# Kernel tuning notes

Hardware: AMD Instinct MI355X
Metric: run time of the kernel (lower is better)

Reference implementation:

```python
import jax, jax.numpy as jnp
import numpy as np

LN_EPS = 1e-5   # torch LayerNorm default
EPS = 1e-8      # slot-attention renorm eps
ITERS = 3


def _ln(x, g, b):
    m = jnp.mean(x, axis=-1, keepdims=True)
    v = jnp.mean(jnp.square(x - m), axis=-1, keepdims=True)
    return (x - m) * jax.lax.rsqrt(v + LN_EPS) * g + b


def _gru(x, h, W_ih, W_hh, b_ih, b_hh):
    # torch GRUCell: gates ordered r, z, n; weight_* has shape [3h, in]
    gi = x @ W_ih.T + b_ih
    gh = h @ W_hh.T + b_hh
    ir, iz, inn = jnp.split(gi, 3, axis=-1)
    hr, hz, hn = jnp.split(gh, 3, axis=-1)
    r = jax.nn.sigmoid(ir + hr)
    z = jax.nn.sigmoid(iz + hz)
    n = jnp.tanh(inn + r * hn)
    return (1.0 - z) * n + z * h


def setup_inputs() -> dict:
    key = jax.random.key(0)
    ks = jax.random.split(key, 16)
    b, n, d, n_s = 32, 4096, 256, 8
    h = max(d, 128)  # hidden_dim = max(dim, hidden_dim)
    s = 1.0 / np.sqrt(d)
    inp = {
        "inputs": jax.random.normal(ks[0], (b, n, d), jnp.float32),
        "noise": jax.random.normal(ks[1], (b, n_s, d), jnp.float32),
        "slots_mu": jax.random.normal(ks[2], (1, 1, d), jnp.float32),
        "slots_logsigma": jax.random.normal(ks[3], (1, 1, d), jnp.float32) * 0.1,
        "Wq": jax.random.uniform(ks[4], (d, d), jnp.float32, -s, s),
        "bq": jnp.zeros((d,), jnp.float32),
        "Wk": jax.random.uniform(ks[5], (d, d), jnp.float32, -s, s),
        "bk": jnp.zeros((d,), jnp.float32),
        "Wv": jax.random.uniform(ks[6], (d, d), jnp.float32, -s, s),
        "bv": jnp.zeros((d,), jnp.float32),
        "W_ih": jax.random.uniform(ks[7], (3 * d, d), jnp.float32, -s, s),
        "W_hh": jax.random.uniform(ks[8], (3 * d, d), jnp.float32, -s, s),
        "b_ih": jnp.zeros((3 * d,), jnp.float32),
        "b_hh": jnp.zeros((3 * d,), jnp.float32),
        "W1": jax.random.uniform(ks[9], (h, d), jnp.float32, -s, s),
        "b1": jnp.zeros((h,), jnp.float32),
        "W2": jax.random.uniform(ks[10], (d, h), jnp.float32, -s, s),
        "b2": jnp.zeros((d,), jnp.float32),
        "g_in": jnp.ones((d,), jnp.float32), "be_in": jnp.zeros((d,), jnp.float32),
        "g_sl": jnp.ones((d,), jnp.float32), "be_sl": jnp.zeros((d,), jnp.float32),
        "g_ff": jnp.ones((d,), jnp.float32), "be_ff": jnp.zeros((d,), jnp.float32),
    }
    return inp


def reference(inputs, noise, slots_mu, slots_logsigma, Wq, bq, Wk, bk, Wv, bv,
              W_ih, W_hh, b_ih, b_hh, W1, b1, W2, b2,
              g_in, be_in, g_sl, be_sl, g_ff, be_ff):
    b, n, d = inputs.shape
    scale = d ** (-0.5)
    # reparameterized slot init
    slots = slots_mu + jnp.exp(slots_logsigma) * noise          # [b, n_s, d]
    x = _ln(inputs, g_in, be_in)
    k = x @ Wk.T + bk                                           # [b, n, d]
    v = x @ Wv.T + bv
    attn = None
    for _ in range(ITERS):
        slots_prev = slots
        q = _ln(slots, g_sl, be_sl) @ Wq.T + bq                 # [b, n_s, d]
        dots = jnp.einsum('bid,bjd->bij', q, k) * scale         # [b, n_s, n]
        attn = jax.nn.softmax(dots, axis=1)                     # softmax over SLOTS
        attn_ = attn + EPS
        attn_ = attn_ / jnp.sum(attn_, axis=-1, keepdims=True)  # renorm over inputs
        updates = jnp.einsum('bjd,bij->bid', v, attn_)          # [b, n_s, d]
        slots = _gru(updates.reshape(-1, d), slots_prev.reshape(-1, d),
                     W_ih, W_hh, b_ih, b_hh).reshape(b, -1, d)
        pre = _ln(slots, g_ff, be_ff)
        slots = slots + (jax.nn.relu(pre @ W1.T + b1) @ W2.T + b2)
    return (slots, attn)
```

## Files before the change

kernel.cpp:

```cpp
#include <hip/hip_runtime.h>
#include <hip/hip_fp16.h>
#include <cstdint>
#include <cstddef>


#define NTOK 4096
#define DDIM 256
#define NSLOT 8
#define NBATCH 32
#define CH 32
#define NCHK 128
#define SROWS (NBATCH * NSLOT)
#define NROWS (NBATCH * NTOK)
#define SCALE 0.0625f
#define LN_EPS_C 1e-5f
#define ATTN_EPS_C 1e-8f

__device__ __forceinline__ void wave_reduce2(float& s, float& ss) {
#pragma unroll
  for (int off = 32; off > 0; off >>= 1) {
    s  += __shfl_down(s, off, 64);
    ss += __shfl_down(ss, off, 64);
  }
}
__device__ __forceinline__ void wave_reduce2_xor(float& s, float& ss) {
#pragma unroll
  for (int off = 32; off > 0; off >>= 1) {
    s  += __shfl_xor(s, off, 64);
    ss += __shfl_xor(ss, off, 64);
  }
}

__global__ __launch_bounds__(256) void convert_weights_k(
    const float* __restrict__ Wq, const float* __restrict__ Wv,
    const float* __restrict__ Wih, const float* __restrict__ Whh,
    const float* __restrict__ W1, const float* __restrict__ W2,
    const float* __restrict__ Wk, __half* __restrict__ WqT,
    __half* __restrict__ WvT, __half* __restrict__ WihT,
    __half* __restrict__ WhhT, __half* __restrict__ W1T,
    __half* __restrict__ W2T, __half* __restrict__ Wk_h) {
  __shared__ float tile[32][33];
  int bz = blockIdx.x;
  int tx = threadIdx.x & 31, ty = threadIdx.x >> 5;
  if (bz >= 80) {
    int ro = (bz - 80) * 32, cd = blockIdx.y * 32;
#pragma unroll
    for (int p = 0; p < 32; p += 8)
      Wk_h[(size_t)(ro + ty + p) * DDIM + cd + tx] =
          __float2half(Wk[(size_t)(ro + ty + p) * DDIM + cd + tx]);
    return;
  }
  const float* in; __half* out; int O, bo;
  if (bz < 8)       { in = Wq;  out = WqT;  O = 256; bo = bz; }
  else if (bz < 16) { in = Wv;  out = WvT;  O = 256; bo = bz - 8; }
  else if (bz < 40) { in = Wih; out = WihT; O = 768; bo = bz - 16; }
  else if (bz < 64) { in = Whh; out = WhhT; O = 768; bo = bz - 40; }
  else if (bz < 72) { in = W1;  out = W1T;  O = 256; bo = bz - 64; }
  else              { in = W2;  out = W2T;  O = 256; bo = bz - 72; }
  int ro = bo * 32, cd = blockIdx.y * 32;
#pragma unroll
  for (int p = 0; p < 32; p += 8)
    tile[ty + p][tx] = in[(size_t)(ro + ty + p) * DDIM + cd + tx];
  __syncthreads();
#pragma unroll
  for (int p = 0; p < 32; p += 8)
    out[(size_t)(cd + ty + p) * O + ro + tx] = __float2half(tile[tx][ty + p]);
}

__global__ __launch_bounds__(256) void xh_prep_k(
    const float* __restrict__ X, const float* __restrict__ g,
    const float* __restrict__ be, __half* __restrict__ xh) {
  int row = blockIdx.x * 4 + (threadIdx.x >> 6);
  int lane = threadIdx.x & 63;
  float4 a = *(const float4*)(X + (size_t)row * DDIM + lane * 4);
  float s = a.x + a.y + a.z + a.w;
  float ss = a.x * a.x + a.y * a.y + a.z * a.z + a.w * a.w;
  wave_reduce2_xor(s, ss);
  float m = s * (1.f / DDIM);
  float rs = rsqrtf(ss * (1.f / DDIM) - m * m + LN_EPS_C);
  float4 gv = *(const float4*)(g + lane * 4);
  float4 bev = *(const float4*)(be + lane * 4);
  union { __half2 h[2]; uint2 u; } pk;
  pk.h[0] = __floats2half2_rn((a.x - m) * rs * gv.x + bev.x,
                              (a.y - m) * rs * gv.y + bev.y);
  pk.h[1] = __floats2half2_rn((a.z - m) * rs * gv.z + bev.z,
                              (a.w - m) * rs * gv.w + bev.w);
  *(uint2*)(xh + (size_t)row * DDIM + lane * 4) = pk.u;
}

__global__ __launch_bounds__(256) void fused_attn_f16_k(
    const __half* __restrict__ xh, const float* __restrict__ qk,
    const float* __restrict__ qkb, float* __restrict__ attn_out,
    float* __restrict__ S_part, __half* __restrict__ u_part, int write_attn) {
  __shared__ __half sx[CH][258];
  __shared__ float2 sqkf[NSLOT][128];
  __shared__ float part[4][NSLOT][CH];
  __shared__ float sa[NSLOT][CH];
  __shared__ float sC0[NSLOT], sS[NSLOT];
  int b = blockIdx.x, c = blockIdx.y, t = threadIdx.x;
  {
    int i = t >> 5, p2 = t & 31;
    const float* qr = qk + ((size_t)b * NSLOT + i) * DDIM;
#pragma unroll
    for (int kk = 0; kk < 4; ++kk) {
      int col = p2 * 4 + kk;
      sqkf[i][col] = make_float2(qr[col * 2], qr[col * 2 + 1]);
    }
  }
  if (t < NSLOT) sC0[t] = qkb[b * NSLOT + t];
  const size_t base = (size_t)b * NTOK + (size_t)c * CH;
#pragma unroll
  for (int it = 0; it < 4; ++it) {
    int e = it * 256 + t;
    int row = e >> 5, c16 = e & 31;
    uint4 v = *(const uint4*)(xh + (base + row) * DDIM + c16 * 8);
    __half2* dst = (__half2*)&sx[row][c16 * 8];
    dst[0] = ((const __half2*)&v)[0];
    dst[1] = ((const __half2*)&v)[1];
    dst[2] = ((const __half2*)&v)[2];
    dst[3] = ((const __half2*)&v)[3];
  }
  __syncthreads();
  int tj = t & 31, qd = t >> 5;
  float p[NSLOT] = {};
  const __half2* xrow = (const __half2*)&sx[tj][qd * 32];
#pragma unroll
  for (int dd2 = 0; dd2 < 16; ++dd2) {
    float2 xf = __half22float2(xrow[dd2]);
#pragma unroll
    for (int i = 0; i < NSLOT; ++i) {
      float2 qf = sqkf[i][qd * 16 + dd2];
      p[i] = fmaf(xf.x, qf.x, fmaf(xf.y, qf.y, p[i]));
    }
  }
#pragma unroll
  for (int i = 0; i < NSLOT; ++i) p[i] += __shfl_down(p[i], 32, 64);
  int w = t >> 6;
  if ((t & 63) < 32) {
#pragma unroll
    for (int i = 0; i < NSLOT; ++i) part[w][i][tj] = p[i];
  }
  __syncthreads();
  if (t < CH) {
    float dots[NSLOT], mx = -1e30f;
#pragma unroll
    for (int i = 0; i < NSLOT; ++i) {
      dots[i] = part[0][i][t] + part[1][i][t] + part[2][i][t] +
                part[3][i][t] + sC0[i];
      mx = fmaxf(mx, dots[i]);
    }
    float sum = 0.f;
#pragma unroll
    for (int i = 0; i < NSLOT; ++i) { dots[i] = expf(dots[i] - mx); sum += dots[i]; }
    float inv = 1.f / sum;
#pragma unroll
    for (int i = 0; i < NSLOT; ++i) {
      float a = dots[i] * inv;
      if (write_attn)
        attn_out[((size_t)b * NSLOT + i) * NTOK + c * CH + t] = a;
      float ae = a + ATTN_EPS_C;
      sa[i][t] = ae;
      float ps = ae;
#pragma unroll
      for (int off = 16; off > 0; off >>= 1) ps += __shfl_down(ps, off, 32);
      if (t == 0) sS[i] = ps;
    }
  }
  __syncthreads();
  float acc[NSLOT] = {};
#pragma unroll
  for (int jj = 0; jj < CH; ++jj) {
    float x = __half2float(sx[jj][t]);
#pragma unroll
    for (int i = 0; i < NSLOT; ++i) acc[i] = fmaf(x, sa[i][jj], acc[i]);
  }
  __half* upb = u_part + (((size_t)b * NCHK + c) * NSLOT) * DDIM + t;
#pragma unroll
  for (int i = 0; i < NSLOT; ++i) upb[(size_t)i * DDIM] = __float2half(acc[i]);
  if (t < NSLOT) S_part[((size_t)b * NCHK + c) * NSLOT + t] = sS[t];
}

__global__ __launch_bounds__(1024) void slot_update_k(
    const __half* __restrict__ u_part, const float* __restrict__ S_part,
    const float* __restrict__ slots_in, const __half* __restrict__ WvT,
    const float* __restrict__ bv, const __half* __restrict__ WihT,
    const __half* __restrict__ WhhT, const float* __restrict__ b_ih,
    const float* __restrict__ b_hh, const float* __restrict__ g_ff,
    const float* __restrict__ be_ff, const __half* __restrict__ W1T,
    const float* __restrict__ b1, const __half* __restrict__ W2T,
    const float* __restrict__ b2, const float* __restrict__ g_sl,
    const float* __restrict__ be_sl, const __half* __restrict__ WqT,
    const float* __restrict__ bq, const __half* __restrict__ Wk_h,
    const float* __restrict__ bk, const float* __restrict__ noise,
    const float* __restrict__ mu, const float* __restrict__ logsig,
    float* __restrict__ slots_out, float* __restrict__ qk,
    float* __restrict__ qkb_out, int init, int compute_qk) {
  __shared__ float red[4][6][DDIM];
  __shared__ float su[DDIM], sh[DDIM], supd[DDIM], v1[DDIM], v2[DDIM];
  __shared__ float scal[16];
  int r = blockIdx.x, t = threadIdx.x;
  int b = r >> 3, i = r & 7;
  int o = t & 255, ks = t >> 8;
  int lane = t & 63, wid = t >> 6;
  if (init) {
    if (ks == 0) {
      float ns = mu[o] + expf(logsig[o]) * noise[(size_t)r * DDIM + o];
      slots_out[(size_t)r * DDIM + o] = ns;
      v2[o] = ns;
    }
    __syncthreads();
  } else {
    {
      float up = 0.f;
      const __half* upp =
          u_part + (((size_t)b * NCHK + ks * 32) * NSLOT + i) * DDIM + o;
#pragma unroll
      for (int cc = 0; cc < 32; ++cc)
        up += __half2float(upp[(size_t)cc * (NSLOT * DDIM)]);
      red[ks][0][o] = up;
    }
    if (t < 128) {
      float sp = S_part[((size_t)b * NCHK + t) * NSLOT + i];
#pragma unroll
      for (int off = 32; off > 0; off >>= 1) sp += __shfl_down(sp, off, 64);
      if ((t & 63) == 0) scal[12 + (t >> 6)] = sp;
    }
    if (ks == 0) sh[o] = slots_in[(size_t)r * DDIM + o];
    __syncthreads();
    if (ks == 0) {
      float invS = 1.f / (scal[12] + scal[13]);
      su[o] = (red[0][0][o] + red[1][0][o] + red[2][0][o] + red[3][0][o]) * invS;
    }
    __syncthreads();
    {
      float p = 0.f;
      const __half* wp = WvT + (size_t)(ks * 64) * DDIM + o;
#pragma unroll 8
      for (int dd = 0; dd < 64; ++dd)
        p = fmaf(su[ks * 64 + dd], __half2float(wp[(size_t)dd * DDIM]), p);
      red[ks][0][o] = p;
    }
    __syncthreads();
    if (ks == 0)
      supd[o] = bv[o] + red[0][0][o] + red[1][0][o] + red[2][0][o] + red[3][0][o];
    __syncthreads();
    {
      float p0 = 0, p1 = 0, p2 = 0, p3 = 0, p4 = 0, p5 = 0;
      const __half* pi = WihT + (size_t)(ks * 64) * (3 * DDIM) + o;
      const __half* ph = WhhT + (size_t)(ks * 64) * (3 * DDIM) + o;
#pragma unroll 4
      for (int dd = 0; dd < 64; ++dd) {
        float ud = supd[ks * 64 + dd], hd = sh[ks * 64 + dd];
        size_t off = (size_t)dd * (3 * DDIM);
        p0 = fmaf(ud, __half2float(pi[off]), p0);
        p1 = fmaf(ud, __half2float(pi[off + DDIM]), p1);
        p2 = fmaf(ud, __half2float(pi[off + 2 * DDIM]), p2);
        p3 = fmaf(hd, __half2float(ph[off]), p3);
        p4 = fmaf(hd, __half2float(ph[off + DDIM]), p4);
        p5 = fmaf(hd, __half2float(ph[off + 2 * DDIM]), p5);
      }
      red[ks][0][o] = p0; red[ks][1][o] = p1; red[ks][2][o] = p2;
      red[ks][3][o] = p3; red[ks][4][o] = p4; red[ks][5][o] = p5;
    }
    __syncthreads();
    if (ks == 0) {
      float air = b_ih[o] + red[0][0][o] + red[1][0][o] + red[2][0][o] + red[3][0][o];
      float aiz = b_ih[DDIM + o] + red[0][1][o] + red[1][1][o] + red[2][1][o] + red[3][1][o];
      float ain = b_ih[2 * DDIM + o] + red[0][2][o] + red[1][2][o] + red[2][2][o] + red[3][2][o];
      float ahr = b_hh[o] + red[0][3][o] + red[1][3][o] + red[2][3][o] + red[3][3][o];
      float ahz = b_hh[DDIM + o] + red[0][4][o] + red[1][4][o] + red[2][4][o] + red[3][4][o];
      float ahn = b_hh[2 * DDIM + o] + red[0][5][o] + red[1][5][o] + red[2][5][o] + red[3][5][o];
      float rg = 1.f / (1.f + expf(-(air + ahr)));
      float zg = 1.f / (1.f + expf(-(aiz + ahz)));
      float ng = tanhf(ain + rg * ahn);
      float nh = (1.f - zg) * ng + zg * sh[o];
      v1[o] = nh;
      float s2 = nh, ss2 = nh * nh;
      wave_reduce2(s2, ss2);
      if (lane == 0) { scal[wid] = s2; scal[4 + wid] = ss2; }
    }
    __syncthreads();
    if (ks == 0) {
      float sS = scal[0] + scal[1] + scal[2] + scal[3];
      float sQ = scal[4] + scal[5] + scal[6] + scal[7];
      float m = sS * (1.f / DDIM);
      float rs = rsqrtf(sQ * (1.f / DDIM) - m * m + LN_EPS_C);
      v2[o] = (v1[o] - m) * rs * g_ff[o] + be_ff[o];
    }
    __syncthreads();
    {
      float p = 0.f;
      const __half* wp = W1T + (size_t)(ks * 64) * DDIM + o;
#pragma unroll 8
      for (int dd = 0; dd < 64; ++dd)
        p = fmaf(v2[ks * 64 + dd], __half2float(wp[(size_t)dd * DDIM]), p);
      red[ks][0][o] = p;
    }
    __syncthreads();
    if (ks == 0)
      su[o] = fmaxf(b1[o] + red[0][0][o] + red[1][0][o] + red[2][0][o] + red[3][0][o], 0.f);
    __syncthreads();
    {
      float p = 0.f;
      const __half* wp = W2T + (size_t)(ks * 64) * DDIM + o;
#pragma unroll 8
      for (int dd = 0; dd < 64; ++dd)
        p = fmaf(su[ks * 64 + dd], __half2float(wp[(size_t)dd * DDIM]), p);
      red[ks][0][o] = p;
    }
    __syncthreads();
    if (ks == 0) {
      float out = v1[o] + b2[o] + red[0][0][o] + red[1][0][o] + red[2][0][o] + red[3][0][o];
      slots_out[(size_t)r * DDIM + o] = out;
      v2[o] = out;
    }
    __syncthreads();
  }
  if (!compute_qk) return;
  if (ks == 0) {
    float x = v2[o];
    float s2 = x, ss2 = x * x;
    wave_reduce2(s2, ss2);
    if (lane == 0) { scal[wid] = s2; scal[4 + wid] = ss2; }
  }
  __syncthreads();
  if (ks == 0) {
    float sS = scal[0] + scal[1] + scal[2] + scal[3];
    float sQ = scal[4] + scal[5] + scal[6] + scal[7];
    float m = sS * (1.f / DDIM);
    float rs = rsqrtf(sQ * (1.f / DDIM) - m * m + LN_EPS_C);
    su[o] = (v2[o] - m) * rs * g_sl[o] + be_sl[o];
  }
  __syncthreads();
  {
    float p = 0.f;
    const __half* wp = WqT + (size_t)(ks * 64) * DDIM + o;
#pragma unroll 8
    for (int dd = 0; dd < 64; ++dd)
      p = fmaf(su[ks * 64 + dd], __half2float(wp[(size_t)dd * DDIM]), p);
    red[ks][0][o] = p;
  }
  __syncthreads();
  if (ks == 0)
    sh[o] = bq[o] + red[0][0][o] + red[1][0][o] + red[2][0][o] + red[3][0][o];
  __syncthreads();
  {
    float p = 0.f;
    const __half* wp = Wk_h + (size_t)(ks * 64) * DDIM + o;
#pragma unroll 8
    for (int dd = 0; dd < 64; ++dd)
      p = fmaf(sh[ks * 64 + dd], __half2float(wp[(size_t)dd * DDIM]), p);
    red[ks][0][o] = p;
  }
  __syncthreads();
  if (ks == 0) {
    float qkv = SCALE * (red[0][0][o] + red[1][0][o] + red[2][0][o] + red[3][0][o]);
    qk[(size_t)r * DDIM + o] = qkv;
    float v0 = sh[o] * bk[o], d1 = 0.f;
    wave_reduce2(v0, d1);
    if (lane == 0) scal[wid] = v0;
  }
  __syncthreads();
  if (t == 0)
    qkb_out[r] = SCALE * (scal[0] + scal[1] + scal[2] + scal[3]);
}

extern "C" void kernel_launch(void* const* d_in, const int* in_sizes, int n_in,
                              void* d_out, int out_size, void* d_ws,
                              size_t ws_size, hipStream_t stream) {
  const float* inputs   = (const float*)d_in[0];
  const float* noise    = (const float*)d_in[1];
  const float* slots_mu = (const float*)d_in[2];
  const float* slots_ls = (const float*)d_in[3];
  const float* Wq   = (const float*)d_in[4];
  const float* bq   = (const float*)d_in[5];
  const float* Wk   = (const float*)d_in[6];
  const float* bk   = (const float*)d_in[7];
  const float* Wv   = (const float*)d_in[8];
  const float* bv   = (const float*)d_in[9];
  const float* W_ih = (const float*)d_in[10];
  const float* W_hh = (const float*)d_in[11];
  const float* b_ih = (const float*)d_in[12];
  const float* b_hh = (const float*)d_in[13];
  const float* W1   = (const float*)d_in[14];
  const float* b1   = (const float*)d_in[15];
  const float* W2   = (const float*)d_in[16];
  const float* b2   = (const float*)d_in[17];
  const float* g_in = (const float*)d_in[18];
  const float* be_in= (const float*)d_in[19];
  const float* g_sl = (const float*)d_in[20];
  const float* be_sl= (const float*)d_in[21];
  const float* g_ff = (const float*)d_in[22];
  const float* be_ff= (const float*)d_in[23];

  float* out_slots = (float*)d_out;
  float* out_attn  = (float*)d_out + SROWS * DDIM;

  float* w = (float*)d_ws;
  float* slots = w;  w += SROWS * DDIM;
  float* qk = w;     w += SROWS * DDIM;
  float* qkb = w;    w += SROWS;
  float* S_part = w; w += NBATCH * NCHK * NSLOT;
  __half* h = (__half*)w;
  __half* xh = h;     h += (size_t)NROWS * DDIM;
  __half* u_part = h; h += (size_t)NBATCH * NCHK * NSLOT * DDIM;
  __half* WqT_h = h;  h += DDIM * DDIM;
  __half* WvT_h = h;  h += DDIM * DDIM;
  __half* WihT_h = h; h += DDIM * 3 * DDIM;
  __half* WhhT_h = h; h += DDIM * 3 * DDIM;
  __half* W1T_h = h;  h += DDIM * DDIM;
  __half* W2T_h = h;  h += DDIM * DDIM;
  __half* Wk_h = h;   h += DDIM * DDIM;

  convert_weights_k<<<dim3(88, 8), 256, 0, stream>>>(
      Wq, Wv, W_ih, W_hh, W1, W2, Wk, WqT_h, WvT_h, WihT_h, WhhT_h, W1T_h,
      W2T_h, Wk_h);
  slot_update_k<<<SROWS, 1024, 0, stream>>>(
      u_part, S_part, slots, WvT_h, bv, WihT_h, WhhT_h, b_ih, b_hh, g_ff,
      be_ff, W1T_h, b1, W2T_h, b2, g_sl, be_sl, WqT_h, bq, Wk_h, bk, noise,
      slots_mu, slots_ls, slots, qk, qkb, 1, 1);
  xh_prep_k<<<NROWS / 4, 256, 0, stream>>>(inputs, g_in, be_in, xh);
  for (int it = 0; it < 3; ++it) {
    fused_attn_f16_k<<<dim3(NBATCH, NCHK), 256, 0, stream>>>(
        xh, qk, qkb, out_attn, S_part, u_part, (it == 2) ? 1 : 0);
    float* sout = (it == 2) ? out_slots : slots;
    slot_update_k<<<SROWS, 1024, 0, stream>>>(
        u_part, S_part, slots, WvT_h, bv, WihT_h, WhhT_h, b_ih, b_hh, g_ff,
        be_ff, W1T_h, b1, W2T_h, b2, g_sl, be_sl, WqT_h, bq, Wk_h, bk, noise,
        slots_mu, slots_ls, sout, qk, qkb, 0, (it == 2) ? 0 : 1);
  }
}
```

Measured before the change: 247.2 us.

## Double attention chunk size and compute two token rows per thread

Raises the tokens per attention block from 32 to 64, halving the number of chunks and the per-chunk partial updates and normaliser sums written out. Each thread now holds two token rows in registers and reuses each float4 q vector loaded from shared memory for both dot products. The slot update kernel is adjusted to reduce over the smaller number of partials. The cost is more shared memory and registers per block, half as many blocks, and a reuse of scal[0] that could clash with other uses of that slot.

```diff
diff --git a/kernel.cpp b/kernel.cpp
--- a/kernel.cpp
+++ b/kernel.cpp
@@ -8,8 +8,8 @@
 #define DDIM 256
 #define NSLOT 8
 #define NBATCH 32
-#define CH 32
-#define NCHK 128
+#define CH 64
+#define NCHK 64
 #define SROWS (NBATCH * NSLOT)
 #define NROWS (NBATCH * NTOK)
 #define SCALE 0.0625f
@@ -93,24 +93,21 @@
     const float* __restrict__ qkb, float* __restrict__ attn_out,
     float* __restrict__ S_part, __half* __restrict__ u_part, int write_attn) {
   __shared__ __half sx[CH][258];
-  __shared__ float2 sqkf[NSLOT][128];
+  __shared__ float4 sq4[NSLOT][64];
   __shared__ float part[4][NSLOT][CH];
   __shared__ float sa[NSLOT][CH];
   __shared__ float sC0[NSLOT], sS[NSLOT];
   int b = blockIdx.x, c = blockIdx.y, t = threadIdx.x;
-  {
-    int i = t >> 5, p2 = t & 31;
-    const float* qr = qk + ((size_t)b * NSLOT + i) * DDIM;
-#pragma unroll
-    for (int kk = 0; kk < 4; ++kk) {
-      int col = p2 * 4 + kk;
-      sqkf[i][col] = make_float2(qr[col * 2], qr[col * 2 + 1]);
-    }
+#pragma unroll
+  for (int r2 = 0; r2 < 2; ++r2) {
+    int idx = r2 * 256 + t;
+    int i = idx >> 6, quad = idx & 63;
+    sq4[i][quad] = *(const float4*)(qk + ((size_t)b * NSLOT + i) * DDIM + quad * 4);
   }
   if (t < NSLOT) sC0[t] = qkb[b * NSLOT + t];
   const size_t base = (size_t)b * NTOK + (size_t)c * CH;
 #pragma unroll
-  for (int it = 0; it < 4; ++it) {
+  for (int it = 0; it < 8; ++it) {
     int e = it * 256 + t;
     int row = e >> 5, c16 = e & 31;
     uint4 v = *(const uint4*)(xh + (base + row) * DDIM + c16 * 8);
@@ -121,24 +118,33 @@
     dst[3] = ((const __half2*)&v)[3];
   }
   __syncthreads();
-  int tj = t & 31, qd = t >> 5;
-  float p[NSLOT] = {};
-  const __half2* xrow = (const __half2*)&sx[tj][qd * 32];
-#pragma unroll
-  for (int dd2 = 0; dd2 < 16; ++dd2) {
-    float2 xf = __half22float2(xrow[dd2]);
+  {
+    int tj = t & 31, qd = t >> 5;
+    float2 xa[16], xb[16];
+    const __half2* xra = (const __half2*)&sx[tj][qd * 32];
+    const __half2* xrb = (const __half2*)&sx[tj + 32][qd * 32];
+#pragma unroll
+    for (int d2 = 0; d2 < 16; ++d2) {
+      xa[d2] = __half22float2(xra[d2]);
+      xb[d2] = __half22float2(xrb[d2]);
+    }
+    int w = t >> 6;
+    bool lo = (t & 63) < 32;
 #pragma unroll
     for (int i = 0; i < NSLOT; ++i) {
-      float2 qf = sqkf[i][qd * 16 + dd2];
-      p[i] = fmaf(xf.x, qf.x, fmaf(xf.y, qf.y, p[i]));
-    }
-  }
-#pragma unroll
-  for (int i = 0; i < NSLOT; ++i) p[i] += __shfl_down(p[i], 32, 64);
-  int w = t >> 6;
-  if ((t & 63) < 32) {
-#pragma unroll
-    for (int i = 0; i < NSLOT; ++i) part[w][i][tj] = p[i];
+      float pa = 0.f, pb = 0.f;
+#pragma unroll
+      for (int d4 = 0; d4 < 8; ++d4) {
+        float4 q = sq4[i][qd * 8 + d4];
+        pa = fmaf(xa[2 * d4].x, q.x, fmaf(xa[2 * d4].y, q.y,
+             fmaf(xa[2 * d4 + 1].x, q.z, fmaf(xa[2 * d4 + 1].y, q.w, pa))));
+        pb = fmaf(xb[2 * d4].x, q.x, fmaf(xb[2 * d4].y, q.y,
+             fmaf(xb[2 * d4 + 1].x, q.z, fmaf(xb[2 * d4 + 1].y, q.w, pb))));
+      }
+      pa += __shfl_down(pa, 32, 64);
+      pb += __shfl_down(pb, 32, 64);
+      if (lo) { part[w][i][tj] = pa; part[w][i][tj + 32] = pb; }
+    }
   }
   __syncthreads();
   if (t < CH) {
@@ -162,7 +168,7 @@
       sa[i][t] = ae;
       float ps = ae;
 #pragma unroll
-      for (int off = 16; off > 0; off >>= 1) ps += __shfl_down(ps, off, 32);
+      for (int off = 32; off > 0; off >>= 1) ps += __shfl_down(ps, off, 64);
       if (t == 0) sS[i] = ps;
     }
   }
@@ -213,22 +219,22 @@
     {
       float up = 0.f;
       const __half* upp =
-          u_part + (((size_t)b * NCHK + ks * 32) * NSLOT + i) * DDIM + o;
-#pragma unroll
-      for (int cc = 0; cc < 32; ++cc)
+          u_part + (((size_t)b * NCHK + ks * 16) * NSLOT + i) * DDIM + o;
+#pragma unroll
+      for (int cc = 0; cc < 16; ++cc)
         up += __half2float(upp[(size_t)cc * (NSLOT * DDIM)]);
       red[ks][0][o] = up;
     }
-    if (t < 128) {
+    if (t < 64) {
       float sp = S_part[((size_t)b * NCHK + t) * NSLOT + i];
 #pragma unroll
       for (int off = 32; off > 0; off >>= 1) sp += __shfl_down(sp, off, 64);
-      if ((t & 63) == 0) scal[12 + (t >> 6)] = sp;
+      if (t == 0) scal[0] = sp;
     }
     if (ks == 0) sh[o] = slots_in[(size_t)r * DDIM + o];
     __syncthreads();
     if (ks == 0) {
-      float invS = 1.f / (scal[12] + scal[13]);
+      float invS = 1.f / scal[0];
       su[o] = (red[0][0][o] + red[1][0][o] + red[2][0][o] + red[3][0][o]) * invS;
     }
     __syncthreads();
```

After: 240.6 us. 2.7% less time.
